# Kernel tuning notes

Hardware: AMD Instinct MI355X
Metric: run time of the kernel (lower is better)

Reference implementation:

```python
import jax, jax.numpy as jnp
import numpy as np

N_NODES = 50000
N_EDGES = 800000
IN_FEATS = 256
HIDDEN = 128
OUT_FEATS = 64


def setup_inputs() -> dict:
    key = jax.random.key(0)
    k1, k2, k3, k4, k5 = jax.random.split(key, 5)
    x = jax.random.normal(k1, (N_NODES, IN_FEATS), dtype=jnp.float32)
    src = jax.random.randint(k2, (N_EDGES,), 0, N_NODES, dtype=jnp.int64)
    dst = jax.random.randint(k3, (N_EDGES,), 0, N_NODES, dtype=jnp.int64)
    # Glorot-ish init for linear weights (DGL GraphConv uses xavier_uniform)
    W1 = jax.random.normal(k4, (IN_FEATS, HIDDEN), dtype=jnp.float32) / np.sqrt(IN_FEATS)
    W2 = jax.random.normal(k5, (HIDDEN, OUT_FEATS), dtype=jnp.float32) / np.sqrt(HIDDEN)
    b1 = jnp.zeros((HIDDEN,), dtype=jnp.float32)
    b2 = jnp.zeros((OUT_FEATS,), dtype=jnp.float32)
    return {"x": x, "src": src, "dst": dst, "W1": W1, "b1": b1, "W2": W2, "b2": b2}


def _norms(src, dst, n_nodes):
    ones = jnp.ones(src.shape[0], dtype=jnp.float32)
    deg_out = jax.ops.segment_sum(ones, src, num_segments=n_nodes)
    deg_in = jax.ops.segment_sum(ones, dst, num_segments=n_nodes)
    # DGL clamps zero degrees to 1 to avoid inf
    norm_src = jnp.power(jnp.clip(deg_out, 1.0, None), -0.5)  # [N]
    norm_dst = jnp.power(jnp.clip(deg_in, 1.0, None), -0.5)   # [N]
    return norm_src, norm_dst


def _gcn_layer(h, W, b, src, dst, norm_src, norm_dst, n_nodes):
    # norm='both': D_dst^{-1/2} A D_src^{-1/2} (h W) + b
    # multiply by W first (in_feats >= out_feats -> cheaper aggregation)
    m = (h * norm_src[:, None]) @ W            # [N, out]
    agg = jax.ops.segment_sum(m[src], dst, num_segments=n_nodes)  # [N, out]
    return agg * norm_dst[:, None] + b


def reference(x, src, dst, W1, b1, W2, b2):
    n = x.shape[0]
    norm_src, norm_dst = _norms(src, dst, n)
    h = _gcn_layer(x, W1, b1, src, dst, norm_src, norm_dst, n)
    h = jax.nn.relu(h)
    h = _gcn_layer(h, W2, b2, src, dst, norm_src, norm_dst, n)
    return h
```

## Files before the change

kernel.cpp:

```cpp
#include <hip/hip_runtime.h>

#define N_NODES 50000
#define N_EDGES 800000
#define IN_FEATS 256
#define HIDDEN 128
#define OUT_FEATS 64

#define NB 8192
#define NRANGE 7
#define NBT (NRANGE * NB)
#define NCHUNK 64
#define EPC 12500

typedef _Float16 f16;
typedef _Float16 f16x2 __attribute__((ext_vector_type(2)));
typedef _Float16 f16x8 __attribute__((ext_vector_type(8)));
typedef float f32x4 __attribute__((ext_vector_type(4)));

__global__ __launch_bounds__(256) void hist_kernel(
    const int* __restrict__ src, const int* __restrict__ dst,
    int* __restrict__ hist_src, int* __restrict__ hist_dst) {
  __shared__ int ls[NB];
  __shared__ int ld2[NB];
  const int r = blockIdx.x % NRANGE;
  const int c = blockIdx.x / NRANGE;
  const int lo = r * NB;
  for (int i = threadIdx.x; i < NB; i += 256) {
    ls[i] = 0;
    ld2[i] = 0;
  }
  __syncthreads();
  const int4* s4 = (const int4*)(src + c * EPC);
  const int4* d4 = (const int4*)(dst + c * EPC);
  for (int i = threadIdx.x; i < EPC / 4; i += 256) {
    int4 s = s4[i];
    int4 d = d4[i];
    unsigned b;
    b = (unsigned)(s.x - lo); if (b < NB) atomicAdd(&ls[b], 1);
    b = (unsigned)(s.y - lo); if (b < NB) atomicAdd(&ls[b], 1);
    b = (unsigned)(s.z - lo); if (b < NB) atomicAdd(&ls[b], 1);
    b = (unsigned)(s.w - lo); if (b < NB) atomicAdd(&ls[b], 1);
    b = (unsigned)(d.x - lo); if (b < NB) atomicAdd(&ld2[b], 1);
    b = (unsigned)(d.y - lo); if (b < NB) atomicAdd(&ld2[b], 1);
    b = (unsigned)(d.z - lo); if (b < NB) atomicAdd(&ld2[b], 1);
    b = (unsigned)(d.w - lo); if (b < NB) atomicAdd(&ld2[b], 1);
  }
  __syncthreads();
  int* hs = hist_src + (long)c * NBT + lo;
  int* hd = hist_dst + (long)c * NBT + lo;
  for (int i = threadIdx.x; i < NB; i += 256) {
    hs[i] = ls[i];
    hd[i] = ld2[i];
  }
}

__global__ __launch_bounds__(256) void reduce_kernel(
    const int* __restrict__ hist_src, int* __restrict__ hist_dst,
    int* __restrict__ deg_in, float* __restrict__ norm_src,
    float* __restrict__ norm_dst, int* __restrict__ partial) {
  int n = blockIdx.x * 256 + threadIdx.x;
  int run = 0;
  if (n < N_NODES) {
    int so = 0;
#pragma unroll 8
    for (int c = 0; c < NCHUNK; ++c) so += hist_src[(long)c * NBT + n];
    norm_src[n] = rsqrtf((float)max(so, 1));
#pragma unroll 8
    for (int c = 0; c < NCHUNK; ++c) {
      int t = hist_dst[(long)c * NBT + n];
      hist_dst[(long)c * NBT + n] = run;
      run += t;
    }
    deg_in[n] = run;
    norm_dst[n] = rsqrtf((float)max(run, 1));
  }
  __shared__ int sd[256];
  sd[threadIdx.x] = run;
  __syncthreads();
  for (int s = 128; s > 0; s >>= 1) {
    if (threadIdx.x < s) sd[threadIdx.x] += sd[threadIdx.x + s];
    __syncthreads();
  }
  if (threadIdx.x == 0) partial[blockIdx.x] = sd[0];
}

__global__ __launch_bounds__(256) void scan2(int* __restrict__ partial,
                                             int nb) {
  __shared__ int sd[256];
  int v = (threadIdx.x < nb) ? partial[threadIdx.x] : 0;
  sd[threadIdx.x] = v;
  __syncthreads();
  for (int off = 1; off < 256; off <<= 1) {
    int t = sd[threadIdx.x] +
            ((threadIdx.x >= off) ? sd[threadIdx.x - off] : 0);
    __syncthreads();
    sd[threadIdx.x] = t;
    __syncthreads();
  }
  if (threadIdx.x < nb) partial[threadIdx.x] = sd[threadIdx.x] - v;
}

__global__ __launch_bounds__(256) void scan3(const int* __restrict__ deg,
                                             const int* __restrict__ partial,
                                             int* __restrict__ rowptr) {
  __shared__ int sd[256];
  int i = blockIdx.x * 256 + threadIdx.x;
  int v = (i < N_NODES) ? deg[i] : 0;
  sd[threadIdx.x] = v;
  __syncthreads();
  for (int off = 1; off < 256; off <<= 1) {
    int t = sd[threadIdx.x] +
            ((threadIdx.x >= off) ? sd[threadIdx.x - off] : 0);
    __syncthreads();
    sd[threadIdx.x] = t;
    __syncthreads();
  }
  if (i < N_NODES) rowptr[i] = partial[blockIdx.x] + sd[threadIdx.x] - v;
  if (blockIdx.x == 0 && threadIdx.x == 0) rowptr[N_NODES] = N_EDGES;
}

__global__ __launch_bounds__(256) void fill_csr(
    const int* __restrict__ src, const int* __restrict__ dst,
    const int* __restrict__ rowptr, const int* __restrict__ pref,
    int* __restrict__ col) {
  __shared__ int cur[NB];
  const int r = blockIdx.x % NRANGE;
  const int c = blockIdx.x / NRANGE;
  const int lo = r * NB;
  for (int i = threadIdx.x; i < NB; i += 256) {
    int n = lo + i;
    cur[i] = (n < N_NODES) ? rowptr[n] + pref[(long)c * NBT + n] : 0;
  }
  __syncthreads();
  const int4* s4 = (const int4*)(src + c * EPC);
  const int4* d4 = (const int4*)(dst + c * EPC);
  for (int i = threadIdx.x; i < EPC / 4; i += 256) {
    int4 s = s4[i];
    int4 d = d4[i];
    unsigned b;
    b = (unsigned)(d.x - lo);
    if (b < NB) col[atomicAdd(&cur[b], 1)] = s.x;
    b = (unsigned)(d.y - lo);
    if (b < NB) col[atomicAdd(&cur[b], 1)] = s.y;
    b = (unsigned)(d.z - lo);
    if (b < NB) col[atomicAdd(&cur[b], 1)] = s.z;
    b = (unsigned)(d.w - lo);
    if (b < NB) col[atomicAdd(&cur[b], 1)] = s.w;
  }
}

__global__ __launch_bounds__(256) void wtrans(const float* __restrict__ W1,
                                              const float* __restrict__ W2,
                                              f16* __restrict__ W1T,
                                              f16* __restrict__ W2T) {
  int i = blockIdx.x * 256 + threadIdx.x;
  if (i < 128 * 256) {
    int n = i >> 8, k = i & 255;
    W1T[i] = (f16)W1[k * 128 + n];
  } else if (i < 128 * 256 + 64 * 128) {
    int j = i - 128 * 256;
    int n = j >> 7, k = j & 127;
    W2T[j] = (f16)W2[k * 64 + n];
  }
}

template <int K, int NC, bool FP32IN>
__global__ __launch_bounds__(256) void gemm_mfma(
    const void* __restrict__ Xv, const f16* __restrict__ WT,
    const float* __restrict__ ns, f16* __restrict__ Mout) {
  constexpr int KI = K / 32;
  constexpr int NT = NC / 16;
  const int wave = threadIdx.x >> 6;
  const int lane = threadIdx.x & 63;
  const int m = lane & 15;
  const int q = lane >> 4;
  const int wrow0 = blockIdx.x * 128 + wave * 32;

  const int ra0 = min(wrow0 + m, N_NODES - 1);
  const int ra1 = min(wrow0 + 16 + m, N_NODES - 1);
  const float s0 = FP32IN ? ns[ra0] : 0.f;
  const float s1 = FP32IN ? ns[ra1] : 0.f;

  f32x4 acc[2][NT];
#pragma unroll
  for (int ab = 0; ab < 2; ++ab)
#pragma unroll
    for (int t = 0; t < NT; ++t) acc[ab][t] = (f32x4){0.f, 0.f, 0.f, 0.f};

#pragma unroll
  for (int ki = 0; ki < KI; ++ki) {
    const int kbase = ki * 32 + q * 8;
    f16x8 a0, a1;
    if (FP32IN) {
      const float* X = (const float*)Xv;
      const float* p0 = X + (long)ra0 * K + kbase;
      const float* p1 = X + (long)ra1 * K + kbase;
      float4 u0 = *(const float4*)p0;
      float4 u1 = *(const float4*)(p0 + 4);
      float4 w0 = *(const float4*)p1;
      float4 w1 = *(const float4*)(p1 + 4);
      a0[0] = (f16)(u0.x * s0); a0[1] = (f16)(u0.y * s0);
      a0[2] = (f16)(u0.z * s0); a0[3] = (f16)(u0.w * s0);
      a0[4] = (f16)(u1.x * s0); a0[5] = (f16)(u1.y * s0);
      a0[6] = (f16)(u1.z * s0); a0[7] = (f16)(u1.w * s0);
      a1[0] = (f16)(w0.x * s1); a1[1] = (f16)(w0.y * s1);
      a1[2] = (f16)(w0.z * s1); a1[3] = (f16)(w0.w * s1);
      a1[4] = (f16)(w1.x * s1); a1[5] = (f16)(w1.y * s1);
      a1[6] = (f16)(w1.z * s1); a1[7] = (f16)(w1.w * s1);
    } else {
      const f16* X = (const f16*)Xv;
      a0 = *(const f16x8*)(X + (long)ra0 * K + kbase);
      a1 = *(const f16x8*)(X + (long)ra1 * K + kbase);
    }
#pragma unroll
    for (int t = 0; t < NT; ++t) {
      f16x8 b = *(const f16x8*)(WT + (long)(t * 16 + m) * K + kbase);
      acc[0][t] =
          __builtin_amdgcn_mfma_f32_16x16x32_f16(a0, b, acc[0][t], 0, 0, 0);
      acc[1][t] =
          __builtin_amdgcn_mfma_f32_16x16x32_f16(a1, b, acc[1][t], 0, 0, 0);
    }
  }

#pragma unroll
  for (int ab = 0; ab < 2; ++ab)
#pragma unroll
    for (int r = 0; r < 4; ++r) {
      int row = wrow0 + ab * 16 + q * 4 + r;
      if (row < N_NODES) {
#pragma unroll
        for (int t = 0; t < NT; ++t)
          Mout[(long)row * NC + t * 16 + m] = (f16)acc[ab][t][r];
      }
    }
}

__global__ __launch_bounds__(256) void gather1_kernel(
    const f16* __restrict__ M, const int* __restrict__ rowptr,
    const int* __restrict__ col, const float* __restrict__ nd,
    const float* __restrict__ ns, const float* __restrict__ b,
    f16* __restrict__ out) {
  constexpr int LPR = 16;
  constexpr int EPW = 64 / LPR;
  const int wave = threadIdx.x >> 6;
  const int lane = threadIdx.x & 63;
  const int g = lane / LPR;
  const int t = lane % LPR;
  const int n = blockIdx.x * 4 + wave;
  if (n >= N_NODES) return;
  const int beg = rowptr[n];
  const int end = rowptr[n + 1];

  float acc[8];
#pragma unroll
  for (int j = 0; j < 8; ++j) acc[j] = 0.f;

  int i = beg + g;
  for (; i + EPW < end; i += 2 * EPW) {
    int s0 = col[i];
    int s1 = col[i + EPW];
    f16x8 v0 = *(const f16x8*)(M + (long)s0 * HIDDEN + t * 8);
    f16x8 v1 = *(const f16x8*)(M + (long)s1 * HIDDEN + t * 8);
#pragma unroll
    for (int j = 0; j < 8; ++j) acc[j] += (float)v0[j] + (float)v1[j];
  }
  if (i < end) {
    int s0 = col[i];
    f16x8 v0 = *(const f16x8*)(M + (long)s0 * HIDDEN + t * 8);
#pragma unroll
    for (int j = 0; j < 8; ++j) acc[j] += (float)v0[j];
  }

#pragma unroll
  for (int m2 = LPR; m2 < 64; m2 <<= 1)
#pragma unroll
    for (int j = 0; j < 8; ++j) acc[j] += __shfl_xor(acc[j], m2, 64);

  if (g == 0) {
    float s = nd[n];
    float sn = ns[n];
    float4 bb0 = *(const float4*)(b + t * 8);
    float4 bb1 = *(const float4*)(b + t * 8 + 4);
    f16x8 o;
    o[0] = (f16)(fmaxf(acc[0] * s + bb0.x, 0.f) * sn);
    o[1] = (f16)(fmaxf(acc[1] * s + bb0.y, 0.f) * sn);
    o[2] = (f16)(fmaxf(acc[2] * s + bb0.z, 0.f) * sn);
    o[3] = (f16)(fmaxf(acc[3] * s + bb0.w, 0.f) * sn);
    o[4] = (f16)(fmaxf(acc[4] * s + bb1.x, 0.f) * sn);
    o[5] = (f16)(fmaxf(acc[5] * s + bb1.y, 0.f) * sn);
    o[6] = (f16)(fmaxf(acc[6] * s + bb1.z, 0.f) * sn);
    o[7] = (f16)(fmaxf(acc[7] * s + bb1.w, 0.f) * sn);
    *(f16x8*)(out + (long)n * HIDDEN + t * 8) = o;
  }
}

__global__ __launch_bounds__(256) void gather2_kernel(
    const f16* __restrict__ M, const int* __restrict__ rowptr,
    const int* __restrict__ col, const float* __restrict__ nd,
    const float* __restrict__ b, float* __restrict__ out) {
  constexpr int LPR = 8;
  constexpr int EPW = 64 / LPR;
  const int wave = threadIdx.x >> 6;
  const int lane = threadIdx.x & 63;
  const int g = lane / LPR;
  const int t = lane % LPR;
  const int n = blockIdx.x * 4 + wave;
  if (n >= N_NODES) return;
  const int beg = rowptr[n];
  const int end = rowptr[n + 1];

  float acc[8];
#pragma unroll
  for (int j = 0; j < 8; ++j) acc[j] = 0.f;

  int i = beg + g;
  for (; i + EPW < end; i += 2 * EPW) {
    int s0 = col[i];
    int s1 = col[i + EPW];
    f16x8 v0 = *(const f16x8*)(M + (long)s0 * OUT_FEATS + t * 8);
    f16x8 v1 = *(const f16x8*)(M + (long)s1 * OUT_FEATS + t * 8);
#pragma unroll
    for (int j = 0; j < 8; ++j) acc[j] += (float)v0[j] + (float)v1[j];
  }
  if (i < end) {
    int s0 = col[i];
    f16x8 v0 = *(const f16x8*)(M + (long)s0 * OUT_FEATS + t * 8);
#pragma unroll
    for (int j = 0; j < 8; ++j) acc[j] += (float)v0[j];
  }

#pragma unroll
  for (int m2 = LPR; m2 < 64; m2 <<= 1)
#pragma unroll
    for (int j = 0; j < 8; ++j) acc[j] += __shfl_xor(acc[j], m2, 64);

  if (g == 0) {
    float s = nd[n];
    float4 bb0 = *(const float4*)(b + t * 8);
    float4 bb1 = *(const float4*)(b + t * 8 + 4);
    float4 o0, o1;
    o0.x = acc[0] * s + bb0.x;
    o0.y = acc[1] * s + bb0.y;
    o0.z = acc[2] * s + bb0.z;
    o0.w = acc[3] * s + bb0.w;
    o1.x = acc[4] * s + bb1.x;
    o1.y = acc[5] * s + bb1.y;
    o1.z = acc[6] * s + bb1.z;
    o1.w = acc[7] * s + bb1.w;
    *(float4*)(out + (long)n * OUT_FEATS + t * 8) = o0;
    *(float4*)(out + (long)n * OUT_FEATS + t * 8 + 4) = o1;
  }
}

extern "C" void kernel_launch(void* const* d_in, const int* in_sizes, int n_in,
                              void* d_out, int out_size, void* d_ws,
                              size_t ws_size, hipStream_t stream) {
  const float* x = (const float*)d_in[0];
  const int* src = (const int*)d_in[1];
  const int* dst = (const int*)d_in[2];
  const float* W1 = (const float*)d_in[3];
  const float* b1 = (const float*)d_in[4];
  const float* W2 = (const float*)d_in[5];
  const float* b2 = (const float*)d_in[6];
  float* out = (float*)d_out;

  int* wi = (int*)d_ws;
  int* partial = wi;
  int* rowptr = wi + 256;
  int* deg_in = wi + 50260;
  int* col = wi + 100260;
  float* wf = (float*)d_ws + 900260;
  float* norm_src = wf;
  float* norm_dst = wf + 50000;
  f16* fh = (f16*)(wf + 100000);
  f16* W1T = fh;
  f16* W2T = fh + 128 * 256;
  f16* m1 = fh + 128 * 256 + 64 * 128;
  f16* h1p = m1 + (long)50048 * 128;
  f16* m2 = h1p + (long)50048 * 128;

  int* hist_src = (int*)m1;
  int* hist_dst = hist_src + (long)NCHUNK * NBT;

  const int nb_nodes = (N_NODES + 255) / 256;

  hist_kernel<<<NRANGE * NCHUNK, 256, 0, stream>>>(src, dst, hist_src,
                                                   hist_dst);
  reduce_kernel<<<nb_nodes, 256, 0, stream>>>(hist_src, hist_dst, deg_in,
                                              norm_src, norm_dst, partial);
  scan2<<<1, 256, 0, stream>>>(partial, nb_nodes);
  scan3<<<nb_nodes, 256, 0, stream>>>(deg_in, partial, rowptr);
  fill_csr<<<NRANGE * NCHUNK, 256, 0, stream>>>(src, dst, rowptr, hist_dst,
                                                col);
  wtrans<<<(128 * 256 + 64 * 128 + 255) / 256, 256, 0, stream>>>(W1, W2, W1T,
                                                                 W2T);

  gemm_mfma<IN_FEATS, HIDDEN, true>
      <<<(N_NODES + 127) / 128, 256, 0, stream>>>(x, W1T, norm_src, m1);
  gather1_kernel<<<(N_NODES + 3) / 4, 256, 0, stream>>>(m1, rowptr, col,
                                                        norm_dst, norm_src, b1,
                                                        h1p);

  gemm_mfma<HIDDEN, OUT_FEATS, false>
      <<<(N_NODES + 127) / 128, 256, 0, stream>>>(h1p, W2T, norm_src, m2);
  gather2_kernel<<<(N_NODES + 3) / 4, 256, 0, stream>>>(m2, rowptr, col,
                                                        norm_dst, b2, out);
}
```

Before: 249.6 us.

## Pack degree histograms as 16-bit counters and split gathers by feature half

The per-chunk degree histograms now use packed 16-bit counters in LDS and global memory. That lets each block cover 16384 nodes in 4 ranges instead of 7, which cuts redundant edge re-reads and halves histogram traffic. Both gather kernels now launch twice as many blocks, each handling half the feature columns with more edge groups per wave. This raises parallelism for the edge loop at the cost of reading rowptr and col twice. Packed 16-bit counts assume per-chunk degrees stay below 65536, which holds here.

```diff
diff --git a/kernel.cpp b/kernel.cpp
--- a/kernel.cpp
+++ b/kernel.cpp
@@ -6,26 +6,25 @@
 #define HIDDEN 128
 #define OUT_FEATS 64
 
-#define NB 8192
-#define NRANGE 7
+#define NB 16384
+#define NRANGE 4
 #define NBT (NRANGE * NB)
 #define NCHUNK 64
 #define EPC 12500
 
 typedef _Float16 f16;
-typedef _Float16 f16x2 __attribute__((ext_vector_type(2)));
 typedef _Float16 f16x8 __attribute__((ext_vector_type(8)));
 typedef float f32x4 __attribute__((ext_vector_type(4)));
 
 __global__ __launch_bounds__(256) void hist_kernel(
     const int* __restrict__ src, const int* __restrict__ dst,
-    int* __restrict__ hist_src, int* __restrict__ hist_dst) {
-  __shared__ int ls[NB];
-  __shared__ int ld2[NB];
+    unsigned* __restrict__ hist_src, unsigned* __restrict__ hist_dst) {
+  __shared__ unsigned ls[NB / 2];
+  __shared__ unsigned ld2[NB / 2];
   const int r = blockIdx.x % NRANGE;
   const int c = blockIdx.x / NRANGE;
   const int lo = r * NB;
-  for (int i = threadIdx.x; i < NB; i += 256) {
+  for (int i = threadIdx.x; i < NB / 2; i += 256) {
     ls[i] = 0;
     ld2[i] = 0;
   }
@@ -36,39 +35,41 @@
     int4 s = s4[i];
     int4 d = d4[i];
     unsigned b;
-    b = (unsigned)(s.x - lo); if (b < NB) atomicAdd(&ls[b], 1);
-    b = (unsigned)(s.y - lo); if (b < NB) atomicAdd(&ls[b], 1);
-    b = (unsigned)(s.z - lo); if (b < NB) atomicAdd(&ls[b], 1);
-    b = (unsigned)(s.w - lo); if (b < NB) atomicAdd(&ls[b], 1);
-    b = (unsigned)(d.x - lo); if (b < NB) atomicAdd(&ld2[b], 1);
-    b = (unsigned)(d.y - lo); if (b < NB) atomicAdd(&ld2[b], 1);
-    b = (unsigned)(d.z - lo); if (b < NB) atomicAdd(&ld2[b], 1);
-    b = (unsigned)(d.w - lo); if (b < NB) atomicAdd(&ld2[b], 1);
-  }
-  __syncthreads();
-  int* hs = hist_src + (long)c * NBT + lo;
-  int* hd = hist_dst + (long)c * NBT + lo;
-  for (int i = threadIdx.x; i < NB; i += 256) {
+    b = (unsigned)(s.x - lo); if (b < NB) atomicAdd(&ls[b >> 1], 1u << ((b & 1) << 4));
+    b = (unsigned)(s.y - lo); if (b < NB) atomicAdd(&ls[b >> 1], 1u << ((b & 1) << 4));
+    b = (unsigned)(s.z - lo); if (b < NB) atomicAdd(&ls[b >> 1], 1u << ((b & 1) << 4));
+    b = (unsigned)(s.w - lo); if (b < NB) atomicAdd(&ls[b >> 1], 1u << ((b & 1) << 4));
+    b = (unsigned)(d.x - lo); if (b < NB) atomicAdd(&ld2[b >> 1], 1u << ((b & 1) << 4));
+    b = (unsigned)(d.y - lo); if (b < NB) atomicAdd(&ld2[b >> 1], 1u << ((b & 1) << 4));
+    b = (unsigned)(d.z - lo); if (b < NB) atomicAdd(&ld2[b >> 1], 1u << ((b & 1) << 4));
+    b = (unsigned)(d.w - lo); if (b < NB) atomicAdd(&ld2[b >> 1], 1u << ((b & 1) << 4));
+  }
+  __syncthreads();
+  unsigned* hs = hist_src + ((long)c * NBT + lo) / 2;
+  unsigned* hd = hist_dst + ((long)c * NBT + lo) / 2;
+  for (int i = threadIdx.x; i < NB / 2; i += 256) {
     hs[i] = ls[i];
     hd[i] = ld2[i];
   }
 }
 
 __global__ __launch_bounds__(256) void reduce_kernel(
-    const int* __restrict__ hist_src, int* __restrict__ hist_dst,
+    const unsigned* __restrict__ hist_src, unsigned* __restrict__ hist_dst,
     int* __restrict__ deg_in, float* __restrict__ norm_src,
     float* __restrict__ norm_dst, int* __restrict__ partial) {
+  const unsigned short* hs = (const unsigned short*)hist_src;
+  unsigned short* hd = (unsigned short*)hist_dst;
   int n = blockIdx.x * 256 + threadIdx.x;
   int run = 0;
   if (n < N_NODES) {
     int so = 0;
 #pragma unroll 8
-    for (int c = 0; c < NCHUNK; ++c) so += hist_src[(long)c * NBT + n];
+    for (int c = 0; c < NCHUNK; ++c) so += hs[(long)c * NBT + n];
     norm_src[n] = rsqrtf((float)max(so, 1));
 #pragma unroll 8
     for (int c = 0; c < NCHUNK; ++c) {
-      int t = hist_dst[(long)c * NBT + n];
-      hist_dst[(long)c * NBT + n] = run;
+      int t = hd[(long)c * NBT + n];
+      hd[(long)c * NBT + n] = (unsigned short)run;
       run += t;
     }
     deg_in[n] = run;
@@ -121,9 +122,10 @@
 
 __global__ __launch_bounds__(256) void fill_csr(
     const int* __restrict__ src, const int* __restrict__ dst,
-    const int* __restrict__ rowptr, const int* __restrict__ pref,
+    const int* __restrict__ rowptr, const unsigned* __restrict__ pref32,
     int* __restrict__ col) {
   __shared__ int cur[NB];
+  const unsigned short* pref = (const unsigned short*)pref32;
   const int r = blockIdx.x % NRANGE;
   const int c = blockIdx.x / NRANGE;
   const int lo = r * NB;
@@ -240,33 +242,36 @@
     const int* __restrict__ col, const float* __restrict__ nd,
     const float* __restrict__ ns, const float* __restrict__ b,
     f16* __restrict__ out) {
-  constexpr int LPR = 16;
+  constexpr int LPR = 8;
   constexpr int EPW = 64 / LPR;
+  const int hf = blockIdx.x & 1;
+  const int g0 = blockIdx.x >> 1;
   const int wave = threadIdx.x >> 6;
   const int lane = threadIdx.x & 63;
-  const int g = lane / LPR;
+  const int eg = lane / LPR;
   const int t = lane % LPR;
-  const int n = blockIdx.x * 4 + wave;
+  const int n = g0 * 4 + wave;
   if (n >= N_NODES) return;
   const int beg = rowptr[n];
   const int end = rowptr[n + 1];
+  const int fo = hf * 64 + t * 8;
 
   float acc[8];
 #pragma unroll
   for (int j = 0; j < 8; ++j) acc[j] = 0.f;
 
-  int i = beg + g;
+  int i = beg + eg;
   for (; i + EPW < end; i += 2 * EPW) {
     int s0 = col[i];
     int s1 = col[i + EPW];
-    f16x8 v0 = *(const f16x8*)(M + (long)s0 * HIDDEN + t * 8);
-    f16x8 v1 = *(const f16x8*)(M + (long)s1 * HIDDEN + t * 8);
+    f16x8 v0 = *(const f16x8*)(M + (long)s0 * HIDDEN + fo);
+    f16x8 v1 = *(const f16x8*)(M + (long)s1 * HIDDEN + fo);
 #pragma unroll
     for (int j = 0; j < 8; ++j) acc[j] += (float)v0[j] + (float)v1[j];
   }
   if (i < end) {
     int s0 = col[i];
-    f16x8 v0 = *(const f16x8*)(M + (long)s0 * HIDDEN + t * 8);
+    f16x8 v0 = *(const f16x8*)(M + (long)s0 * HIDDEN + fo);
 #pragma unroll
     for (int j = 0; j < 8; ++j) acc[j] += (float)v0[j];
   }
@@ -276,11 +281,11 @@
 #pragma unroll
     for (int j = 0; j < 8; ++j) acc[j] += __shfl_xor(acc[j], m2, 64);
 
-  if (g == 0) {
+  if (eg == 0) {
     float s = nd[n];
     float sn = ns[n];
-    float4 bb0 = *(const float4*)(b + t * 8);
-    float4 bb1 = *(const float4*)(b + t * 8 + 4);
+    float4 bb0 = *(const float4*)(b + fo);
+    float4 bb1 = *(const float4*)(b + fo + 4);
     f16x8 o;
     o[0] = (f16)(fmaxf(acc[0] * s + bb0.x, 0.f) * sn);
     o[1] = (f16)(fmaxf(acc[1] * s + bb0.y, 0.f) * sn);
@@ -290,7 +295,7 @@
     o[5] = (f16)(fmaxf(acc[5] * s + bb1.y, 0.f) * sn);
     o[6] = (f16)(fmaxf(acc[6] * s + bb1.z, 0.f) * sn);
     o[7] = (f16)(fmaxf(acc[7] * s + bb1.w, 0.f) * sn);
-    *(f16x8*)(out + (long)n * HIDDEN + t * 8) = o;
+    *(f16x8*)(out + (long)n * HIDDEN + fo) = o;
   }
 }
 
@@ -298,33 +303,36 @@
     const f16* __restrict__ M, const int* __restrict__ rowptr,
     const int* __restrict__ col, const float* __restrict__ nd,
     const float* __restrict__ b, float* __restrict__ out) {
-  constexpr int LPR = 8;
+  constexpr int LPR = 4;
   constexpr int EPW = 64 / LPR;
+  const int hf = blockIdx.x & 1;
+  const int g0 = blockIdx.x >> 1;
   const int wave = threadIdx.x >> 6;
   const int lane = threadIdx.x & 63;
-  const int g = lane / LPR;
+  const int eg = lane / LPR;
   const int t = lane % LPR;
-  const int n = blockIdx.x * 4 + wave;
+  const int n = g0 * 4 + wave;
   if (n >= N_NODES) return;
   const int beg = rowptr[n];
   const int end = rowptr[n + 1];
+  const int fo = hf * 32 + t * 8;
 
   float acc[8];
 #pragma unroll
   for (int j = 0; j < 8; ++j) acc[j] = 0.f;
 
-  int i = beg + g;
+  int i = beg + eg;
   for (; i + EPW < end; i += 2 * EPW) {
     int s0 = col[i];
     int s1 = col[i + EPW];
-    f16x8 v0 = *(const f16x8*)(M + (long)s0 * OUT_FEATS + t * 8);
-    f16x8 v1 = *(const f16x8*)(M + (long)s1 * OUT_FEATS + t * 8);
+    f16x8 v0 = *(const f16x8*)(M + (long)s0 * OUT_FEATS + fo);
+    f16x8 v1 = *(const f16x8*)(M + (long)s1 * OUT_FEATS + fo);
 #pragma unroll
     for (int j = 0; j < 8; ++j) acc[j] += (float)v0[j] + (float)v1[j];
   }
   if (i < end) {
     int s0 = col[i];
-    f16x8 v0 = *(const f16x8*)(M + (long)s0 * OUT_FEATS + t * 8);
+    f16x8 v0 = *(const f16x8*)(M + (long)s0 * OUT_FEATS + fo);
 #pragma unroll
     for (int j = 0; j < 8; ++j) acc[j] += (float)v0[j];
   }
@@ -334,10 +342,10 @@
 #pragma unroll
     for (int j = 0; j < 8; ++j) acc[j] += __shfl_xor(acc[j], m2, 64);
 
-  if (g == 0) {
+  if (eg == 0) {
     float s = nd[n];
-    float4 bb0 = *(const float4*)(b + t * 8);
-    float4 bb1 = *(const float4*)(b + t * 8 + 4);
+    float4 bb0 = *(const float4*)(b + fo);
+    float4 bb1 = *(const float4*)(b + fo + 4);
     float4 o0, o1;
     o0.x = acc[0] * s + bb0.x;
     o0.y = acc[1] * s + bb0.y;
@@ -347,8 +355,8 @@
     o1.y = acc[5] * s + bb1.y;
     o1.z = acc[6] * s + bb1.z;
     o1.w = acc[7] * s + bb1.w;
-    *(float4*)(out + (long)n * OUT_FEATS + t * 8) = o0;
-    *(float4*)(out + (long)n * OUT_FEATS + t * 8 + 4) = o1;
+    *(float4*)(out + (long)n * OUT_FEATS + fo) = o0;
+    *(float4*)(out + (long)n * OUT_FEATS + fo + 4) = o1;
   }
 }
 
@@ -379,8 +387,8 @@
   f16* h1p = m1 + (long)50048 * 128;
   f16* m2 = h1p + (long)50048 * 128;
 
-  int* hist_src = (int*)m1;
-  int* hist_dst = hist_src + (long)NCHUNK * NBT;
+  unsigned* hist_src = (unsigned*)m1;
+  unsigned* hist_dst = hist_src + (long)NCHUNK * NBT / 2;
 
   const int nb_nodes = (N_NODES + 255) / 256;
 
@@ -397,12 +405,11 @@
 
   gemm_mfma<IN_FEATS, HIDDEN, true>
       <<<(N_NODES + 127) / 128, 256, 0, stream>>>(x, W1T, norm_src, m1);
-  gather1_kernel<<<(N_NODES + 3) / 4, 256, 0, stream>>>(m1, rowptr, col,
-                                                        norm_dst, norm_src, b1,
-                                                        h1p);
+  gather1_kernel<<<2 * ((N_NODES + 3) / 4), 256, 0, stream>>>(
+      m1, rowptr, col, norm_dst, norm_src, b1, h1p);
 
   gemm_mfma<HIDDEN, OUT_FEATS, false>
       <<<(N_NODES + 127) / 128, 256, 0, stream>>>(h1p, W2T, norm_src, m2);
-  gather2_kernel<<<(N_NODES + 3) / 4, 256, 0, stream>>>(m2, rowptr, col,
-                                                        norm_dst, b2, out);
-}
+  gather2_kernel<<<2 * ((N_NODES + 3) / 4), 256, 0, stream>>>(
+      m2, rowptr, col, norm_dst, b2, out);
+}
```

Result: slower. 280.6 us (+12.4%).
